# Performance work log

Hardware: AMD Instinct MI355X
Metric: run time of the kernel (lower is better)

## Reference

```python
import jax, jax.numpy as jnp
import numpy as np
from jax import lax

B_SZ, D_SPEC, P, NC, MLP_D = 4096, 30, 9, 64, 64
L = P * P + 1  # 82 tokens (81 spiral + cls)


def _spiral_idx(patch=P):
    # Replicates Scan.forward's hardcoded assignments_map: center pixel, then
    # concentric rings (top row, right col, bottom row, left col), each of length 2r.
    cen = patch // 2
    rows, cols = [cen], [cen]
    for r in range(1, cen + 1):
        rows += [cen - r] * (2 * r); cols += list(range(cen - r + 1, cen + r + 1))
        rows += list(range(cen - r + 1, cen + r + 1)); cols += [cen + r] * (2 * r)
        rows += [cen + r] * (2 * r); cols += list(range(cen - r, cen + r))
        rows += list(range(cen - r, cen + r)); cols += [cen - r] * (2 * r)
    return np.asarray(rows), np.asarray(cols)

_ROWS, _COLS = _spiral_idx()


def _ln(x, g, b, eps=1e-5):
    m = x.mean(-1, keepdims=True)
    v = ((x - m) ** 2).mean(-1, keepdims=True)
    return (x - m) * lax.rsqrt(v + eps) * g + b


def _bn(x, g, b, m, v, nspatial, eps=1e-5):
    sh = (1, -1) + (1,) * nspatial
    return (x - m.reshape(sh)) * lax.rsqrt(v.reshape(sh) + eps) * g.reshape(sh) + b.reshape(sh)


def setup_inputs():
    key = jax.random.key(0)
    ks = iter(jax.random.split(key, 40))
    def rn(shape, s=0.1):
        return s * jax.random.normal(next(ks), shape, jnp.float32)
    return {
        "input_data": jax.random.normal(next(ks), (B_SZ, 1, D_SPEC, P, P), jnp.float32),
        "w3": rn((8, 1, 3, 3, 3)), "b3": rn((8,)),
        "g3": 1.0 + rn((8,)), "be3": rn((8,)), "m3": jnp.zeros((8,)), "v3": jnp.ones((8,)),
        "w2c": rn((NC, 8 * D_SPEC, 3, 3)), "b2c": rn((NC,)),
        "g2": 1.0 + rn((NC,)), "be2": rn((NC,)), "m2": jnp.zeros((NC,)), "v2": jnp.ones((NC,)),
        "pos_emb": rn((1, L, NC)), "cls_tok": rn((1, 1, NC)),
        "ln1_g": jnp.ones((NC,)), "ln1_b": jnp.zeros((NC,)),
        "Wb": rn((NC, NC)), "bb": rn((NC,)),
        "Wc": rn((NC, NC)), "bc": rn((NC,)),
        "Wd": rn((NC, NC)), "bd": rn((NC,)),
        "delta_p": rn((1, L, NC)), "A_p": rn((L, NC)),
        "Wst": rn((NC, NC)), "bst": rn((NC,)), "bias_st": rn((1, 1, NC)),
        "ln2_g": jnp.ones((NC,)), "ln2_b": jnp.zeros((NC,)),
        "Wm1": rn((NC, MLP_D)), "bm1": rn((MLP_D,)),
        "Wm2": rn((MLP_D, NC)), "bm2": rn((NC,)),
    }


def _forward(input_data, w3, b3, g3, be3, m3, v3, w2c, b2c, g2, be2, m2, v2,
             pos_emb, cls_tok, ln1_g, ln1_b, Wb, bb, Wc, bc, Wd, bd,
             delta_p, A_p, Wst, bst, bias_st, ln2_g, ln2_b, Wm1, bm1, Wm2, bm2):
    b = input_data.shape[0]
    # conv3d (SAME, k=3) + BN(eval) + ReLU
    h = lax.conv_general_dilated(input_data, w3, (1, 1, 1), [(1, 1)] * 3,
                                 dimension_numbers=("NCDHW", "OIDHW", "NCDHW"))
    h = jax.nn.relu(_bn(h + b3[None, :, None, None, None], g3, be3, m3, v3, 3))
    h = h.reshape(b, 8 * D_SPEC, P, P)  # 'b c h w y -> b (c h) w y'
    # conv2d (SAME, k=3) + BN(eval) + ReLU
    h = lax.conv_general_dilated(h, w2c, (1, 1), [(1, 1)] * 2,
                                 dimension_numbers=("NCHW", "OIHW", "NCHW"))
    h = jax.nn.relu(_bn(h + b2c[None, :, None, None], g2, be2, m2, v2, 2))
    # spiral scan gather: [B,C,H,W] -> [B,81,C]
    seq = jnp.transpose(h, (0, 2, 3, 1))[:, _ROWS, _COLS, :]
    tok = jnp.concatenate([jnp.broadcast_to(cls_tok, (b, 1, NC)), seq], axis=1) + pos_emb
    # (emb dropout = identity in eval)
    # --- Residual(LayerNormalize(S6_noC)) ---
    xn = _ln(tok, ln1_g, ln1_b)
    z = jax.nn.sigmoid(xn)
    B0 = xn @ Wb + bb
    C_ = xn @ Wc + bc
    sq = jnp.mean(xn, axis=1, keepdims=True)              # SToken squeeze [B,1,D]
    sq = jax.nn.sigmoid(jax.nn.relu(sq @ Wst + bst))
    T_ = (sq + bias_st) * xn                              # [B,L,D]
    delta = jax.nn.sigmoid(xn @ Wd + bd + delta_p)
    A_ = delta * A_p[None]                                # [B,L,D]
    Bx = delta * B0 * xn                                  # B_ * x fused
    def step(s, inp):
        a, bx, c, t = inp
        s = a * s + bx
        return s, c * s + t
    ins = (jnp.moveaxis(A_, 1, 0), jnp.moveaxis(Bx, 1, 0),
           jnp.moveaxis(C_, 1, 0), jnp.moveaxis(T_, 1, 0))  # [L,B,D]
    _, out = lax.scan(step, jnp.zeros((b, NC), xn.dtype), ins)
    tok = tok + jnp.moveaxis(out, 0, 1) * z               # residual
    # AdaptiveAvgPool1d(1) over seq + squeeze -> [B, D]
    pooled = tok.mean(axis=1)
    # --- Residual(LayerNormalize(MLP_Block)) (dropout = identity) ---
    yn = _ln(pooled, ln2_g, ln2_b)
    mlp = jax.nn.gelu(yn @ Wm1 + bm1, approximate=False) @ Wm2 + bm2
    return pooled + mlp


def reference(input_data, w3, b3, g3, be3, m3, v3, w2c, b2c, g2, be2, m2, v2,
              pos_emb, cls_tok, ln1_g, ln1_b, Wb, bb, Wc, bc, Wd, bd,
              delta_p, A_p, Wst, bst, bias_st, ln2_g, ln2_b, Wm1, bm1, Wm2, bm2):
    return _forward(input_data, w3, b3, g3, be3, m3, v3, w2c, b2c, g2, be2, m2, v2,
                    pos_emb, cls_tok, ln1_g, ln1_b, Wb, bb, Wc, bc, Wd, bd,
                    delta_p, A_p, Wst, bst, bias_st, ln2_g, ln2_b, Wm1, bm1, Wm2, bm2)
```

## Files before the change

### kernel.cpp

```cpp
#include <hip/hip_runtime.h>

typedef unsigned short u16;
typedef unsigned int u32;
typedef __attribute__((ext_vector_type(8))) short bf16x8;
typedef __attribute__((ext_vector_type(4))) float f32x4;
typedef __attribute__((ext_vector_type(4))) int i32x4;

#define DEV __device__ __forceinline__

DEV u16 f2bf(float f){
  unsigned u = __float_as_uint(f);
  u += 0x7fffu + ((u >> 16) & 1u);
  return (u16)(u >> 16);
}
DEV float bf2f(u16 h){ return __uint_as_float(((unsigned)h) << 16); }

DEV int spiral_t(int pix){
  int px = pix / 9, py = pix % 9;
  int dr = px - 4, dc = py - 4;
  int ar = dr < 0 ? -dr : dr, ac = dc < 0 ? -dc : dc;
  int r = ar > ac ? ar : ac;
  if (r == 0) return 0;
  int start = 1 + 4*r*(r-1);
  if (dr == -r && dc >= -r+1) return start + dc + r - 1;
  if (dc == r)  return start + 2*r + dr + r - 1;
  if (dr == r)  return start + 4*r + dc + r;
  return start + 6*r + dr + r;
}

__global__ __launch_bounds__(256) void k_conv3d(const float* __restrict__ x,
    const float* __restrict__ w3, const float* __restrict__ b3,
    const float* __restrict__ g3, const float* __restrict__ be3,
    const float* __restrict__ m3, const float* __restrict__ v3,
    const float* __restrict__ w2c, const float* __restrict__ g2,
    const float* __restrict__ v2,
    u16* __restrict__ h1, u16* __restrict__ Wt2){
  __shared__ float tile[3993];
  __shared__ float wle[216];
  __shared__ float sc[8], sh[8];
  int b = blockIdx.x, tid = threadIdx.x;

  if (b >= 4096){
    int idx = (b - 4096)*256 + tid;
    int kk = idx & 31;
    int o  = (idx >> 5) & 63;
    int tile2 = idx >> 11;
    int dxy = tile2 >> 3;
    int chunk = tile2 & 7;
    int ch = chunk*32 + kk;
    float v = 0.f;
    if (ch < 240){
      float s2 = g2[o] * rsqrtf(v2[o] + 1e-5f);
      v = w2c[(o*240 + ch)*9 + dxy] * s2;
    }
    Wt2[idx] = f2bf(v);
    return;
  }

  for (int i = tid; i < 3993; i += 256) tile[i] = 0.f;
  if (tid < 216) wle[tid] = w3[tid];
  if (tid < 8){
    float s = g3[tid]*rsqrtf(v3[tid]+1e-5f);
    sc[tid] = s;
    sh[tid] = (b3[tid]-m3[tid])*s + be3[tid];
  }
  __syncthreads();
  const float* xin = x + b*2430;
  for (int i = tid; i < 2430; i += 256){
    int dd = i / 81, rem = i % 81;
    int px = rem / 9, py = rem % 9;
    tile[(dd+1)*121 + (px+1)*11 + (py+1)] = xin[i];
  }
  __syncthreads();
  u16* hb = h1 + (size_t)b*19440;

  for (int col = tid; col < 648; col += 256){
    int pix = col >> 3, co = col & 7;
    int px = pix / 9, py = pix % 9;
    const float* base = tile + px*11 + py;
    float wp[27];
    #pragma unroll
    for (int q=0;q<27;q++) wp[q] = wle[co*27+q];
    float scv = sc[co], shv = sh[co];

    float s0[9], s1[9], s2[9];
#define LSL(S, SL)                                                            \
    { const float* tp2 = base + (SL)*121;                                     \
      _Pragma("unroll")                                                       \
      for (int kx=0;kx<3;kx++)                                                \
        _Pragma("unroll")                                                     \
        for (int ky=0;ky<3;ky++) S[kx*3+ky] = tp2[kx*11+ky]; }
#define DOT3(A, SA, SB, SC)                                                   \
    { A = 0.f;                                                                \
      _Pragma("unroll")                                                       \
      for (int q=0;q<9;q++) A = fmaf(SA[q], wp[q], A);                        \
      _Pragma("unroll")                                                       \
      for (int q=0;q<9;q++) A = fmaf(SB[q], wp[9+q], A);                      \
      _Pragma("unroll")                                                       \
      for (int q=0;q<9;q++) A = fmaf(SC[q], wp[18+q], A); }

    LSL(s0, 0); LSL(s1, 1); LSL(s2, 2);
    u16 outv[30];
    #pragma unroll
    for (int d3 = 0; d3 < 30; d3 += 3){
      float a;
      DOT3(a, s0, s1, s2);
      outv[d3] = f2bf(fmaxf(fmaf(a, scv, shv), 0.f));
      LSL(s0, d3+3);
      DOT3(a, s1, s2, s0);
      outv[d3+1] = f2bf(fmaxf(fmaf(a, scv, shv), 0.f));
      LSL(s1, d3+4);
      DOT3(a, s2, s0, s1);
      outv[d3+2] = f2bf(fmaxf(fmaf(a, scv, shv), 0.f));
      LSL(s2, d3+5);
    }
#undef LSL
#undef DOT3
    u32* dst = (u32*)(hb + pix*240 + co*30);
    #pragma unroll
    for (int q=0;q<15;q++) dst[q] = ((u32)outv[2*q+1] << 16) | (u32)outv[2*q];
  }
}

__global__ __launch_bounds__(256, 2) void k_conv2d(const u16* __restrict__ h1,
    const u16* __restrict__ Wt2,
    const float* __restrict__ b2c, const float* __restrict__ g2,
    const float* __restrict__ be2, const float* __restrict__ m2,
    const float* __restrict__ v2,
    const float* __restrict__ pos_emb, const float* __restrict__ cls_tok,
    const float* __restrict__ ln1_g, const float* __restrict__ ln1_b,
    const float* __restrict__ Wst, const float* __restrict__ bst,
    const float* __restrict__ bias_st,
    u16* __restrict__ xn, float* __restrict__ tsum, float* __restrict__ sqs){
  __shared__ __align__(16) char smem[80848];
  const int ZROW = 80352;
  int tid = threadIdx.x;
  int wv = tid >> 6, ln = tid & 63;
  int lq = ln >> 4, lr = ln & 15;
  int img0 = blockIdx.x*2;
  size_t grow0 = (size_t)img0*81;

  int bln = lr*32 + lq*8;

#define LOADB(TAP, C, B)                                                        \
    { const u16* Bt_ = Wt2 + (TAP)*16384 + bln;                                 \
      _Pragma("unroll")                                                         \
      for (int kk=0;kk<2;kk++)                                                  \
        _Pragma("unroll")                                                       \
        for (int j=0;j<4;j++)                                                   \
          B[kk][j] = *(const bf16x8*)(Bt_ + ((C)*2+kk)*2048 + j*512); }

  bf16x8 bB0[2][4], bB1[2][4], bB2[2][4];
  LOADB(0, 0, bB0);
  LOADB(0, 1, bB1);
  LOADB(0, 2, bB2);

  for (int r = tid; r < 162; r += 256)
    *(i32x4*)(smem + r*496 + 480) = (i32x4){0,0,0,0};
  if (tid < 31) *(i32x4*)(smem + ZROW + tid*16) = (i32x4){0,0,0,0};
  {
    const u16* src = h1 + grow0*240;
    for (int idx = tid; idx < 162*30; idx += 256){
      int r = idx / 30, c = idx % 30;
      *(i32x4*)(smem + r*496 + c*16) = *(const i32x4*)(src + idx*8);
    }
  }
  __syncthreads();

  f32x4 acc[3][4];
  #pragma unroll
  for (int i=0;i<3;i++)
    #pragma unroll
    for (int j=0;j<4;j++) acc[i][j] = (f32x4){0.f,0.f,0.f,0.f};

#define CALCADDR(TAP, A0, A1, A13)                                              \
  { int dx = (TAP)/3 - 1, dy = (TAP)%3 - 1;                                     \
    _Pragma("unroll")                                                           \
    for (int rt=0;rt<3;rt++){                                                   \
      int row = (wv*3+rt)*16 + lr;                                              \
      int pix = row % 81;                                                       \
      int px = pix/9, py = pix%9;                                               \
      int px2 = px + dx, py2 = py + dy;                                         \
      bool valid = (row < 162) && ((unsigned)px2 < 9u) && ((unsigned)py2 < 9u); \
      int nrow = (row - pix) + px2*9 + py2;                                     \
      int base = valid ? nrow*496 : ZROW;                                       \
      A0[rt]  = base + lq*16;                                                   \
      A1[rt]  = base + 64 + lq*16;                                              \
      A13[rt] = (lq == 3) ? ZROW : (A1[rt] + 384);                              \
    } }

#define LOADA(C, SA0, SA1, SA13, A0, A1)                                        \
    { _Pragma("unroll")                                                         \
      for (int rt=0;rt<3;rt++){                                                 \
        A0[rt] = *(const bf16x8*)(smem + SA0[rt] + (C)*128);                    \
        A1[rt] = *(const bf16x8*)(smem + ((C)==3 ? SA13[rt]                     \
                                                 : SA1[rt] + (C)*128)); } }

#define DOMFMA(B, A0, A1)                                                       \
    { __builtin_amdgcn_s_setprio(1);                                            \
      _Pragma("unroll")                                                         \
      for (int rt=0;rt<3;rt++)                                                  \
        _Pragma("unroll")                                                       \
        for (int j=0;j<4;j++)                                                   \
          acc[rt][j] = __builtin_amdgcn_mfma_f32_16x16x32_bf16(A0[rt], B[0][j], acc[rt][j], 0, 0, 0); \
      _Pragma("unroll")                                                         \
      for (int rt=0;rt<3;rt++)                                                  \
        _Pragma("unroll")                                                       \
        for (int j=0;j<4;j++)                                                   \
          acc[rt][j] = __builtin_amdgcn_mfma_f32_16x16x32_bf16(A1[rt], B[1][j], acc[rt][j], 0, 0, 0); \
      __builtin_amdgcn_s_setprio(0); }

#define TAPBODY(TAPV, BA, BB, BC)                                               \
  { int ntap_ = (TAPV) < 8 ? (TAPV)+1 : 8;                                      \
    DOMFMA(BA, aAX0, aAX1);                                                     \
    LOADB((TAPV), 3, BA); LOADA(2, aC0, aC1, aC13, aAX0, aAX1);                 \
    DOMFMA(BB, aAY0, aAY1);                                                     \
    LOADB(ntap_, 0, BB); CALCADDR(ntap_, aN0, aN1, aN13);                       \
    LOADA(3, aC0, aC1, aC13, aAY0, aAY1);                                       \
    DOMFMA(BC, aAX0, aAX1);                                                     \
    LOADB(ntap_, 1, BC); LOADA(0, aN0, aN1, aN13, aAX0, aAX1);                  \
    DOMFMA(BA, aAY0, aAY1);                                                     \
    LOADB(ntap_, 2, BA); LOADA(1, aN0, aN1, aN13, aAY0, aAY1);                  \
    _Pragma("unroll")                                                           \
    for (int rt=0;rt<3;rt++){ aC0[rt]=aN0[rt]; aC1[rt]=aN1[rt]; aC13[rt]=aN13[rt]; } }

  int aC0[3], aC1[3], aC13[3];
  int aN0[3], aN1[3], aN13[3];
  bf16x8 aAX0[3], aAX1[3], aAY0[3], aAY1[3];

  CALCADDR(0, aC0, aC1, aC13);
  LOADA(0, aC0, aC1, aC13, aAX0, aAX1);
  LOADA(1, aC0, aC1, aC13, aAY0, aAY1);

  for (int t3 = 0; t3 < 9; t3 += 3){
    TAPBODY(t3+0, bB0, bB1, bB2);
    TAPBODY(t3+1, bB1, bB2, bB0);
    TAPBODY(t3+2, bB2, bB0, bB1);
  }
#undef CALCADDR
#undef LOADB
#undef LOADA
#undef DOMFMA
#undef TAPBODY

  __syncthreads();

  float t2c[4], lg[4], lb[4];
  #pragma unroll
  for (int j=0;j<4;j++){
    int col = j*16 + lr;
    float s2 = g2[col]*rsqrtf(v2[col]+1e-5f);
    t2c[j] = (b2c[col]-m2[col])*s2 + be2[col];
    lg[j] = ln1_g[col]; lb[j] = ln1_b[col];
  }

  float st0[4]={0,0,0,0}, st1[4]={0,0,0,0};
  float sx0[4]={0,0,0,0}, sx1[4]={0,0,0,0};

  #pragma unroll
  for (int rt=0;rt<3;rt++){
    #pragma unroll
    for (int e=0;e<4;e++){
      int row = (wv*3+rt)*16 + lq*4 + e;
      if (row < 162){
        int im = (row >= 81);
        int pix = row - im*81;
        int tsp = spiral_t(pix);
        const float* pe = pos_emb + (1+tsp)*64;
        float y[4], m1 = 0.f, m2v = 0.f;
        #pragma unroll
        for (int j=0;j<4;j++){
          y[j] = fmaxf(acc[rt][j][e] + t2c[j], 0.f) + pe[j*16+lr];
          m1 += y[j]; m2v = fmaf(y[j], y[j], m2v);
        }
        #pragma unroll
        for (int off=1; off<16; off<<=1){
          m1  += __shfl_xor(m1,  off, 64);
          m2v += __shfl_xor(m2v, off, 64);
        }
        float mean = m1*(1.f/64.f);
        float var  = m2v*(1.f/64.f) - mean*mean;
        float rs = rsqrtf(var + 1e-5f);
        u16* dst = xn + ((size_t)(img0+im)*82 + 1 + tsp)*64;
        #pragma unroll
        for (int j=0;j<4;j++){
          float xnv = (y[j]-mean)*rs*lg[j] + lb[j];
          dst[j*16+lr] = f2bf(xnv);
          if (im == 0){ st0[j] += y[j]; sx0[j] += xnv; }
          else        { st1[j] += y[j]; sx1[j] += xnv; }
        }
      }
    }
  }

  #pragma unroll
  for (int j=0;j<4;j++){
    st0[j] += __shfl_xor(st0[j],16,64); st0[j] += __shfl_xor(st0[j],32,64);
    st1[j] += __shfl_xor(st1[j],16,64); st1[j] += __shfl_xor(st1[j],32,64);
    sx0[j] += __shfl_xor(sx0[j],16,64); sx0[j] += __shfl_xor(sx0[j],32,64);
    sx1[j] += __shfl_xor(sx1[j],16,64); sx1[j] += __shfl_xor(sx1[j],32,64);
  }
  float* partT = (float*)smem;
  float* partX = (float*)(smem + 2048);
  float* xsumL = (float*)(smem + 4096);
  if (lq == 0){
    #pragma unroll
    for (int j=0;j<4;j++){
      partT[wv*128 +       j*16+lr] = st0[j];
      partT[wv*128 + 64  + j*16+lr] = st1[j];
      partX[wv*128 +       j*16+lr] = sx0[j];
      partX[wv*128 + 64  + j*16+lr] = sx1[j];
    }
  }
  __syncthreads();
  if (tid < 128){
    int im = tid >> 6, d = tid & 63;
    float tt = partT[im*64+d] + partT[128+im*64+d] + partT[256+im*64+d] + partT[384+im*64+d];
    float xx = partX[im*64+d] + partX[128+im*64+d] + partX[256+im*64+d] + partX[384+im*64+d];
    float clsv = cls_tok[d] + pos_emb[d];
    float c1v = clsv, c2v = clsv*clsv;
    #pragma unroll
    for (int off=1; off<64; off<<=1){ c1v += __shfl_xor(c1v, off, 64); c2v += __shfl_xor(c2v, off, 64); }
    float cm = c1v*(1.f/64.f), cv = c2v*(1.f/64.f) - cm*cm;
    float cxn = (clsv - cm)*rsqrtf(cv + 1e-5f)*ln1_g[d] + ln1_b[d];
    xn[((size_t)(img0+im)*82)*64 + d] = f2bf(cxn);
    tsum[(size_t)(img0+im)*64 + d] = tt + clsv;
    xsumL[im*64 + d] = (xx + cxn) * (1.f/82.f);
  }
  __syncthreads();
  {
    int im = tid >> 7, d2 = tid & 127;
    int d = d2 >> 1, half = d2 & 1;
    float a = 0.f;
    int k0 = half*32;
    #pragma unroll
    for (int k=0;k<32;k++) a = fmaf(xsumL[im*64 + k0+k], Wst[(k0+k)*64+d], a);
    a += __shfl_xor(a, 1, 64);
    if (half == 0){
      a += bst[d];
      a = fmaxf(a, 0.f);
      a = 1.f/(1.f + __expf(-a));
      sqs[(size_t)(img0+im)*64 + d] = a + bias_st[d];
    }
  }
}

__global__ __launch_bounds__(256, 2) void k_fuse(const u16* __restrict__ xn,
    const float* __restrict__ tsum, const float* __restrict__ sqs,
    const float* __restrict__ Wb, const float* __restrict__ Wc, const float* __restrict__ Wd,
    const float* __restrict__ bbv, const float* __restrict__ bcv, const float* __restrict__ bdv,
    const float* __restrict__ delta_p, const float* __restrict__ A_p,
    const float* __restrict__ ln2_g, const float* __restrict__ ln2_b,
    const float* __restrict__ Wm1, const float* __restrict__ bm1,
    const float* __restrict__ Wm2, const float* __restrict__ bm2,
    float* __restrict__ out){
  __shared__ __align__(16) char xnL[96*128];
  __shared__ u16 AxL[96][66], BxL[96][66], CxL[96][66];
  int tid = threadIdx.x;
  int wv = tid >> 6, ln = tid & 63;
  int lq = ln >> 4, lr = ln & 15;
  int b = blockIdx.x;

  bf16x8 bfr[3][2];
  {
    int cc = wv*16 + lr;
    const float* Ws[3] = {Wb, Wc, Wd};
    #pragma unroll
    for (int w=0;w<3;w++)
      #pragma unroll
      for (int kk=0;kk<2;kk++){
        int k0 = kk*32 + lq*8;
        bf16x8 f;
        #pragma unroll
        for (int e=0;e<8;e++) f[e] = (short)f2bf(Ws[w][(k0+e)*64 + cc]);
        bfr[w][kk] = f;
      }
  }

  {
    const u16* src = xn + (size_t)b*82*64;
    for (int idx = tid; idx < 656; idx += 256){
      int r = idx >> 3, c = idx & 7;
      *(i32x4*)(xnL + r*128 + ((c*16) ^ ((r&7)<<4))) = *(const i32x4*)(src + idx*8);
    }
    for (int idx = tid; idx < 112; idx += 256){
      int r = 82 + (idx >> 3), c = idx & 7;
      *(i32x4*)(xnL + r*128 + ((c*16) ^ ((r&7)<<4))) = (i32x4){0,0,0,0};
    }
  }
  __syncthreads();

  f32x4 acc[6][3];
  #pragma unroll
  for (int i=0;i<6;i++)
    #pragma unroll
    for (int w=0;w<3;w++) acc[i][w] = (f32x4){0.f,0.f,0.f,0.f};

  #pragma unroll
  for (int rt=0;rt<6;rt++){
    int row = rt*16 + lr;
    bf16x8 afr[2];
    #pragma unroll
    for (int kk=0;kk<2;kk++)
      afr[kk] = *(const bf16x8*)(xnL + row*128 + ((kk*64 + lq*16) ^ ((row&7)<<4)));
    #pragma unroll
    for (int kk=0;kk<2;kk++)
      #pragma unroll
      for (int w=0;w<3;w++)
        acc[rt][w] = __builtin_amdgcn_mfma_f32_16x16x32_bf16(afr[kk], bfr[w][kk], acc[rt][w], 0, 0, 0);
  }

  {
    int d = wv*16 + lr;
    float bB = bbv[d], bC = bcv[d], bD = bdv[d];
    #pragma unroll
    for (int rt=0;rt<6;rt++){
      #pragma unroll
      for (int e=0;e<4;e++){
        int t = rt*16 + lq*4 + e;
        if (t < 82){
          float B0 = acc[rt][0][e] + bB;
          float Cv = acc[rt][1][e] + bC;
          float Dr = acc[rt][2][e] + bD + delta_p[t*64+d];
          float D  = 1.f/(1.f + __expf(-Dr));
          float xv = bf2f(*(const u16*)(xnL + t*128 + ((d*2) ^ ((t&7)<<4))));
          AxL[t][d] = f2bf(D * A_p[t*64+d]);
          BxL[t][d] = f2bf(D * B0 * xv);
          CxL[t][d] = f2bf(Cv);
        }
      }
    }
  }
  __syncthreads();

  if (wv == 0){
    int d = ln;
    float sq = sqs[(size_t)b*64 + d];
    float s = 0.f, racc = 0.f;
    for (int t = 0; t < 82; t++){
      float a  = bf2f(AxL[t][d]);
      float bx = bf2f(BxL[t][d]);
      float c  = bf2f(CxL[t][d]);
      float xv = bf2f(*(const u16*)(xnL + t*128 + ((d*2) ^ ((t&7)<<4))));
      s = fmaf(a, s, bx);
      float o = fmaf(c, s, sq*xv);
      float z = 1.f/(1.f + __expf(-xv));
      racc = fmaf(o, z, racc);
    }
    float pooled = (tsum[(size_t)b*64 + d] + racc) * (1.f/82.f);
    float s1 = pooled, s2v = pooled*pooled;
    #pragma unroll
    for (int off=32; off>0; off>>=1){ s1 += __shfl_xor(s1, off, 64); s2v += __shfl_xor(s2v, off, 64); }
    float mean = s1*(1.f/64.f), var = s2v*(1.f/64.f) - mean*mean;
    float yn = (pooled - mean)*rsqrtf(var + 1e-5f)*ln2_g[d] + ln2_b[d];
    float a1 = bm1[d];
    for (int k=0;k<64;k++) a1 = fmaf(__shfl(yn, k, 64), Wm1[k*64+d], a1);
    float hg = 0.5f*a1*(1.f + erff(a1*0.70710678118654752f));
    float a2 = bm2[d];
    for (int k=0;k<64;k++) a2 = fmaf(__shfl(hg, k, 64), Wm2[k*64+d], a2);
    out[(size_t)b*64 + d] = pooled + a2;
  }
}

extern "C" void kernel_launch(void* const* d_in, const int* in_sizes, int n_in,
                              void* d_out, int out_size, void* d_ws, size_t ws_size,
                              hipStream_t stream){
  const float* x       = (const float*)d_in[0];
  const float* w3      = (const float*)d_in[1];
  const float* b3      = (const float*)d_in[2];
  const float* g3      = (const float*)d_in[3];
  const float* be3     = (const float*)d_in[4];
  const float* m3      = (const float*)d_in[5];
  const float* v3      = (const float*)d_in[6];
  const float* w2c     = (const float*)d_in[7];
  const float* b2c     = (const float*)d_in[8];
  const float* g2      = (const float*)d_in[9];
  const float* be2     = (const float*)d_in[10];
  const float* m2      = (const float*)d_in[11];
  const float* v2      = (const float*)d_in[12];
  const float* pos_emb = (const float*)d_in[13];
  const float* cls_tok = (const float*)d_in[14];
  const float* ln1_g   = (const float*)d_in[15];
  const float* ln1_b   = (const float*)d_in[16];
  const float* Wb      = (const float*)d_in[17];
  const float* bbv     = (const float*)d_in[18];
  const float* Wc      = (const float*)d_in[19];
  const float* bc      = (const float*)d_in[20];
  const float* Wd      = (const float*)d_in[21];
  const float* bd      = (const float*)d_in[22];
  const float* delta_p = (const float*)d_in[23];
  const float* A_p     = (const float*)d_in[24];
  const float* Wst     = (const float*)d_in[25];
  const float* bst     = (const float*)d_in[26];
  const float* bias_st = (const float*)d_in[27];
  const float* ln2_g   = (const float*)d_in[28];
  const float* ln2_b   = (const float*)d_in[29];
  const float* Wm1     = (const float*)d_in[30];
  const float* bm1     = (const float*)d_in[31];
  const float* Wm2     = (const float*)d_in[32];
  const float* bm2     = (const float*)d_in[33];

  char* ws = (char*)d_ws;
  u16*   h1   = (u16*)ws;
  u16*   Wt2  = (u16*)(ws + 159252480);
  u16*   xnb  = (u16*)(ws + 159571968);
  float* tsum = (float*)(ws + 202563584);
  float* sqs  = (float*)(ws + 203612160);

  k_conv3d<<<4672, 256, 0, stream>>>(x, w3, b3, g3, be3, m3, v3,
                                     w2c, g2, v2, h1, Wt2);
  k_conv2d<<<2048, 256, 0, stream>>>(h1, Wt2, b2c, g2, be2, m2, v2,
                                     pos_emb, cls_tok, ln1_g, ln1_b,
                                     Wst, bst, bias_st, xnb, tsum, sqs);
  k_fuse  <<<4096, 256, 0, stream>>>(xnb, tsum, sqs, Wb, Wc, Wd, bbv, bc, bd,
                                     delta_p, A_p, ln2_g, ln2_b,
                                     Wm1, bm1, Wm2, bm2, (float*)d_out);
}
```

Baseline: 359.3 us.

## Split conv2d K dimension across wave pairs with LDS reduction

Result: slower. 608.0 us (+69.2%).

```diff
diff --git a/kernel.cpp b/kernel.cpp
--- a/kernel.cpp
+++ b/kernel.cpp
@@ -122,7 +122,7 @@
   }
 }
 
-__global__ __launch_bounds__(256, 2) void k_conv2d(const u16* __restrict__ h1,
+__global__ __launch_bounds__(256, 1) void k_conv2d(const u16* __restrict__ h1,
     const u16* __restrict__ Wt2,
     const float* __restrict__ b2c, const float* __restrict__ g2,
     const float* __restrict__ be2, const float* __restrict__ m2,
@@ -137,10 +137,12 @@
   int tid = threadIdx.x;
   int wv = tid >> 6, ln = tid & 63;
   int lq = ln >> 4, lr = ln & 15;
+  int p = wv >> 1, q = wv & 1;
   int img0 = blockIdx.x*2;
   size_t grow0 = (size_t)img0*81;
 
   int bln = lr*32 + lq*8;
+  int c0 = q*2, c1 = q*2 + 1;
 
 #define LOADB(TAP, C, B)                                                        \
     { const u16* Bt_ = Wt2 + (TAP)*16384 + bln;                                 \
@@ -150,10 +152,9 @@
         for (int j=0;j<4;j++)                                                   \
           B[kk][j] = *(const bf16x8*)(Bt_ + ((C)*2+kk)*2048 + j*512); }
 
-  bf16x8 bB0[2][4], bB1[2][4], bB2[2][4];
-  LOADB(0, 0, bB0);
-  LOADB(0, 1, bB1);
-  LOADB(0, 2, bB2);
+  bf16x8 bA[2][4], bB[2][4];
+  LOADB(0, c0, bA);
+  LOADB(0, c1, bB);
 
   for (int r = tid; r < 162; r += 256)
     *(i32x4*)(smem + r*496 + 480) = (i32x4){0,0,0,0};
@@ -167,82 +168,90 @@
   }
   __syncthreads();
 
-  f32x4 acc[3][4];
-  #pragma unroll
-  for (int i=0;i<3;i++)
+  f32x4 acc[6][4];
+  #pragma unroll
+  for (int i=0;i<6;i++)
     #pragma unroll
     for (int j=0;j<4;j++) acc[i][j] = (f32x4){0.f,0.f,0.f,0.f};
 
-#define CALCADDR(TAP, A0, A1, A13)                                              \
+  int aC0[6], aC1[6];
+  bf16x8 afr[6][2];
+
+#define CALCADDR(TAP)                                                           \
   { int dx = (TAP)/3 - 1, dy = (TAP)%3 - 1;                                     \
     _Pragma("unroll")                                                           \
-    for (int rt=0;rt<3;rt++){                                                   \
-      int row = (wv*3+rt)*16 + lr;                                              \
+    for (int rt=0;rt<6;rt++){                                                   \
+      int row = p*96 + rt*16 + lr;                                              \
       int pix = row % 81;                                                       \
       int px = pix/9, py = pix%9;                                               \
       int px2 = px + dx, py2 = py + dy;                                         \
       bool valid = (row < 162) && ((unsigned)px2 < 9u) && ((unsigned)py2 < 9u); \
       int nrow = (row - pix) + px2*9 + py2;                                     \
       int base = valid ? nrow*496 : ZROW;                                       \
-      A0[rt]  = base + lq*16;                                                   \
-      A1[rt]  = base + 64 + lq*16;                                              \
-      A13[rt] = (lq == 3) ? ZROW : (A1[rt] + 384);                              \
+      aC0[rt] = base + lq*16;                                                   \
+      aC1[rt] = base + 64 + lq*16;                                              \
     } }
 
-#define LOADA(C, SA0, SA1, SA13, A0, A1)                                        \
+#define LOADA1(RT, C)                                                           \
+    { afr[RT][0] = *(const bf16x8*)(smem + aC0[RT] + (C)*128);                  \
+      int a1a_ = ((C)==3) ? ((lq==3) ? ZROW : aC1[RT] + 384)                    \
+                          : (aC1[RT] + (C)*128);                                \
+      afr[RT][1] = *(const bf16x8*)(smem + a1a_); }
+
+#define GROUP(B, NC)                                                            \
     { _Pragma("unroll")                                                         \
-      for (int rt=0;rt<3;rt++){                                                 \
-        A0[rt] = *(const bf16x8*)(smem + SA0[rt] + (C)*128);                    \
-        A1[rt] = *(const bf16x8*)(smem + ((C)==3 ? SA13[rt]                     \
-                                                 : SA1[rt] + (C)*128)); } }
-
-#define DOMFMA(B, A0, A1)                                                       \
-    { __builtin_amdgcn_s_setprio(1);                                            \
-      _Pragma("unroll")                                                         \
-      for (int rt=0;rt<3;rt++)                                                  \
+      for (int rt=0;rt<6;rt++){                                                 \
+        __builtin_amdgcn_s_setprio(1);                                          \
         _Pragma("unroll")                                                       \
         for (int j=0;j<4;j++)                                                   \
-          acc[rt][j] = __builtin_amdgcn_mfma_f32_16x16x32_bf16(A0[rt], B[0][j], acc[rt][j], 0, 0, 0); \
-      _Pragma("unroll")                                                         \
-      for (int rt=0;rt<3;rt++)                                                  \
+          acc[rt][j] = __builtin_amdgcn_mfma_f32_16x16x32_bf16(afr[rt][0], B[0][j], acc[rt][j], 0, 0, 0); \
         _Pragma("unroll")                                                       \
         for (int j=0;j<4;j++)                                                   \
-          acc[rt][j] = __builtin_amdgcn_mfma_f32_16x16x32_bf16(A1[rt], B[1][j], acc[rt][j], 0, 0, 0); \
-      __builtin_amdgcn_s_setprio(0); }
-
-#define TAPBODY(TAPV, BA, BB, BC)                                               \
-  { int ntap_ = (TAPV) < 8 ? (TAPV)+1 : 8;                                      \
-    DOMFMA(BA, aAX0, aAX1);                                                     \
-    LOADB((TAPV), 3, BA); LOADA(2, aC0, aC1, aC13, aAX0, aAX1);                 \
-    DOMFMA(BB, aAY0, aAY1);                                                     \
-    LOADB(ntap_, 0, BB); CALCADDR(ntap_, aN0, aN1, aN13);                       \
-    LOADA(3, aC0, aC1, aC13, aAY0, aAY1);                                       \
-    DOMFMA(BC, aAX0, aAX1);                                                     \
-    LOADB(ntap_, 1, BC); LOADA(0, aN0, aN1, aN13, aAX0, aAX1);                  \
-    DOMFMA(BA, aAY0, aAY1);                                                     \
-    LOADB(ntap_, 2, BA); LOADA(1, aN0, aN1, aN13, aAY0, aAY1);                  \
-    _Pragma("unroll")                                                           \
-    for (int rt=0;rt<3;rt++){ aC0[rt]=aN0[rt]; aC1[rt]=aN1[rt]; aC13[rt]=aN13[rt]; } }
-
-  int aC0[3], aC1[3], aC13[3];
-  int aN0[3], aN1[3], aN13[3];
-  bf16x8 aAX0[3], aAX1[3], aAY0[3], aAY1[3];
-
-  CALCADDR(0, aC0, aC1, aC13);
-  LOADA(0, aC0, aC1, aC13, aAX0, aAX1);
-  LOADA(1, aC0, aC1, aC13, aAY0, aAY1);
-
-  for (int t3 = 0; t3 < 9; t3 += 3){
-    TAPBODY(t3+0, bB0, bB1, bB2);
-    TAPBODY(t3+1, bB1, bB2, bB0);
-    TAPBODY(t3+2, bB2, bB0, bB1);
+          acc[rt][j] = __builtin_amdgcn_mfma_f32_16x16x32_bf16(afr[rt][1], B[1][j], acc[rt][j], 0, 0, 0); \
+        __builtin_amdgcn_s_setprio(0);                                          \
+        LOADA1(rt, NC);                                                         \
+      } }
+
+  CALCADDR(0);
+  #pragma unroll
+  for (int rt=0;rt<6;rt++){ LOADA1(rt, c0); }
+
+  for (int tap = 0; tap < 9; tap++){
+    int ntap = (tap < 8) ? tap + 1 : 8;
+    GROUP(bA, c1);
+    LOADB(ntap, c0, bA);
+    CALCADDR(ntap);
+    GROUP(bB, c0);
+    LOADB(ntap, c1, bB);
   }
 #undef CALCADDR
 #undef LOADB
-#undef LOADA
-#undef DOMFMA
-#undef TAPBODY
-
+#undef LOADA1
+#undef GROUP
+
+  __syncthreads();
+  float* ex = (float*)smem;
+  int rtw0 = q ? 0 : 3;
+  #pragma unroll
+  for (int k=0;k<3;k++){
+    int rt = rtw0 + k;
+    #pragma unroll
+    for (int e=0;e<4;e++)
+      #pragma unroll
+      for (int j=0;j<4;j++)
+        ex[p*6144 + (rt*16 + lq*4 + e)*64 + j*16 + lr] = acc[rt][j][e];
+  }
+  __syncthreads();
+  int rtr0 = q ? 3 : 0;
+  #pragma unroll
+  for (int k=0;k<3;k++){
+    int rt = rtr0 + k;
+    #pragma unroll
+    for (int e=0;e<4;e++)
+      #pragma unroll
+      for (int j=0;j<4;j++)
+        acc[rt][j][e] += ex[p*6144 + (rt*16 + lq*4 + e)*64 + j*16 + lr];
+  }
   __syncthreads();
 
   float t2c[4], lg[4], lb[4];
@@ -258,10 +267,11 @@
   float sx0[4]={0,0,0,0}, sx1[4]={0,0,0,0};
 
   #pragma unroll
-  for (int rt=0;rt<3;rt++){
+  for (int k=0;k<3;k++){
+    int rt = rtr0 + k;
     #pragma unroll
     for (int e=0;e<4;e++){
-      int row = (wv*3+rt)*16 + lq*4 + e;
+      int row = p*96 + rt*16 + lq*4 + e;
       if (row < 162){
         int im = (row >= 81);
         int pix = row - im*81;
```

## Fuse selective-scan and MLP stage into conv2d kernel via shared memory

Applied to the files above, without the earlier changes.

Measured after the change: 361.7 us. Within noise of the previous version (+0.7%).

```diff
diff --git a/kernel.cpp b/kernel.cpp
--- a/kernel.cpp
+++ b/kernel.cpp
@@ -131,9 +131,19 @@
     const float* __restrict__ ln1_g, const float* __restrict__ ln1_b,
     const float* __restrict__ Wst, const float* __restrict__ bst,
     const float* __restrict__ bias_st,
-    u16* __restrict__ xn, float* __restrict__ tsum, float* __restrict__ sqs){
+    const float* __restrict__ Wb, const float* __restrict__ Wc,
+    const float* __restrict__ Wd,
+    const float* __restrict__ bbv, const float* __restrict__ bcv,
+    const float* __restrict__ bdv,
+    const float* __restrict__ delta_p, const float* __restrict__ A_p,
+    const float* __restrict__ ln2_g, const float* __restrict__ ln2_b,
+    const float* __restrict__ Wm1, const float* __restrict__ bm1,
+    const float* __restrict__ Wm2, const float* __restrict__ bm2,
+    float* __restrict__ out){
   __shared__ __align__(16) char smem[80848];
   const int ZROW = 80352;
+  const int TSUML = 24576, SQSL = 25088, AXo = 25600, BXo = 38272, CXo = 50944;
+  const int PTo = 63616, PXo = 65664, XSo = 67712;
   int tid = threadIdx.x;
   int wv = tid >> 6, ln = tid & 63;
   int lq = ln >> 4, lr = ln & 15;
@@ -244,6 +254,12 @@
 #undef TAPBODY
 
   __syncthreads();
+
+  if (tid < 224){
+    int im = tid / 112, r2 = tid % 112;
+    int rr = 82 + (r2 >> 3), c = r2 & 7;
+    *(i32x4*)(smem + im*12288 + rr*128 + ((c*16) ^ ((rr&7)<<4))) = (i32x4){0,0,0,0};
+  }
 
   float t2c[4], lg[4], lb[4];
   #pragma unroll
@@ -281,11 +297,13 @@
         float mean = m1*(1.f/64.f);
         float var  = m2v*(1.f/64.f) - mean*mean;
         float rs = rsqrtf(var + 1e-5f);
-        u16* dst = xn + ((size_t)(img0+im)*82 + 1 + tsp)*64;
+        int trow = 1 + tsp;
+        char* dl = smem + im*12288 + trow*128;
+        int sz = (trow & 7) << 4;
         #pragma unroll
         for (int j=0;j<4;j++){
           float xnv = (y[j]-mean)*rs*lg[j] + lb[j];
-          dst[j*16+lr] = f2bf(xnv);
+          *(u16*)(dl + (((j*16+lr)*2) ^ sz)) = f2bf(xnv);
           if (im == 0){ st0[j] += y[j]; sx0[j] += xnv; }
           else        { st1[j] += y[j]; sx1[j] += xnv; }
         }
@@ -300,9 +318,11 @@
     sx0[j] += __shfl_xor(sx0[j],16,64); sx0[j] += __shfl_xor(sx0[j],32,64);
     sx1[j] += __shfl_xor(sx1[j],16,64); sx1[j] += __shfl_xor(sx1[j],32,64);
   }
-  float* partT = (float*)smem;
-  float* partX = (float*)(smem + 2048);
-  float* xsumL = (float*)(smem + 4096);
+  float* partT = (float*)(smem + PTo);
+  float* partX = (float*)(smem + PXo);
+  float* xsumL = (float*)(smem + XSo);
+  float* tsumL = (float*)(smem + TSUML);
+  float* sqsL  = (float*)(smem + SQSL);
   if (lq == 0){
     #pragma unroll
     for (int j=0;j<4;j++){
@@ -323,8 +343,8 @@
     for (int off=1; off<64; off<<=1){ c1v += __shfl_xor(c1v, off, 64); c2v += __shfl_xor(c2v, off, 64); }
     float cm = c1v*(1.f/64.f), cv = c2v*(1.f/64.f) - cm*cm;
     float cxn = (clsv - cm)*rsqrtf(cv + 1e-5f)*ln1_g[d] + ln1_b[d];
-    xn[((size_t)(img0+im)*82)*64 + d] = f2bf(cxn);
-    tsum[(size_t)(img0+im)*64 + d] = tt + clsv;
+    *(u16*)(smem + im*12288 + d*2) = f2bf(cxn);
+    tsumL[im*64 + d] = tt + clsv;
     xsumL[im*64 + d] = (xx + cxn) * (1.f/82.f);
   }
   __syncthreads();
@@ -340,26 +360,10 @@
       a += bst[d];
       a = fmaxf(a, 0.f);
       a = 1.f/(1.f + __expf(-a));
-      sqs[(size_t)(img0+im)*64 + d] = a + bias_st[d];
-    }
-  }
-}
-
-__global__ __launch_bounds__(256, 2) void k_fuse(const u16* __restrict__ xn,
-    const float* __restrict__ tsum, const float* __restrict__ sqs,
-    const float* __restrict__ Wb, const float* __restrict__ Wc, const float* __restrict__ Wd,
-    const float* __restrict__ bbv, const float* __restrict__ bcv, const float* __restrict__ bdv,
-    const float* __restrict__ delta_p, const float* __restrict__ A_p,
-    const float* __restrict__ ln2_g, const float* __restrict__ ln2_b,
-    const float* __restrict__ Wm1, const float* __restrict__ bm1,
-    const float* __restrict__ Wm2, const float* __restrict__ bm2,
-    float* __restrict__ out){
-  __shared__ __align__(16) char xnL[96*128];
-  __shared__ u16 AxL[96][66], BxL[96][66], CxL[96][66];
-  int tid = threadIdx.x;
-  int wv = tid >> 6, ln = tid & 63;
-  int lq = ln >> 4, lr = ln & 15;
-  int b = blockIdx.x;
+      sqsL[im*64 + d] = a + bias_st[d];
+    }
+  }
+  __syncthreads();
 
   bf16x8 bfr[3][2];
   {
@@ -376,89 +380,83 @@
         bfr[w][kk] = f;
       }
   }
-
-  {
-    const u16* src = xn + (size_t)b*82*64;
-    for (int idx = tid; idx < 656; idx += 256){
-      int r = idx >> 3, c = idx & 7;
-      *(i32x4*)(xnL + r*128 + ((c*16) ^ ((r&7)<<4))) = *(const i32x4*)(src + idx*8);
-    }
-    for (int idx = tid; idx < 112; idx += 256){
-      int r = 82 + (idx >> 3), c = idx & 7;
-      *(i32x4*)(xnL + r*128 + ((c*16) ^ ((r&7)<<4))) = (i32x4){0,0,0,0};
-    }
-  }
-  __syncthreads();
-
-  f32x4 acc[6][3];
-  #pragma unroll
-  for (int i=0;i<6;i++)
-    #pragma unroll
-    for (int w=0;w<3;w++) acc[i][w] = (f32x4){0.f,0.f,0.f,0.f};
-
-  #pragma unroll
-  for (int rt=0;rt<6;rt++){
-    int row = rt*16 + lr;
-    bf16x8 afr[2];
-    #pragma unroll
-    for (int kk=0;kk<2;kk++)
-      afr[kk] = *(const bf16x8*)(xnL + row*128 + ((kk*64 + lq*16) ^ ((row&7)<<4)));
-    #pragma unroll
-    for (int kk=0;kk<2;kk++)
+  u16* AxL = (u16*)(smem + AXo);
+  u16* BxL = (u16*)(smem + BXo);
+  u16* CxL = (u16*)(smem + CXo);
+
+  for (int im = 0; im < 2; im++){
+    const char* xb = smem + im*12288;
+    f32x4 facc[6][3];
+    #pragma unroll
+    for (int i=0;i<6;i++)
       #pragma unroll
-      for (int w=0;w<3;w++)
-        acc[rt][w] = __builtin_amdgcn_mfma_f32_16x16x32_bf16(afr[kk], bfr[w][kk], acc[rt][w], 0, 0, 0);
-  }
-
-  {
-    int d = wv*16 + lr;
-    float bB = bbv[d], bC = bcv[d], bD = bdv[d];
+      for (int w=0;w<3;w++) facc[i][w] = (f32x4){0.f,0.f,0.f,0.f};
+
     #pragma unroll
     for (int rt=0;rt<6;rt++){
+      int row = rt*16 + lr;
+      bf16x8 afr[2];
       #pragma unroll
-      for (int e=0;e<4;e++){
-        int t = rt*16 + lq*4 + e;
-        if (t < 82){
-          float B0 = acc[rt][0][e] + bB;
-          float Cv = acc[rt][1][e] + bC;
-          float Dr = acc[rt][2][e] + bD + delta_p[t*64+d];
-          float D  = 1.f/(1.f + __expf(-Dr));
-          float xv = bf2f(*(const u16*)(xnL + t*128 + ((d*2) ^ ((t&7)<<4))));
-          AxL[t][d] = f2bf(D * A_p[t*64+d]);
-          BxL[t][d] = f2bf(D * B0 * xv);
-          CxL[t][d] = f2bf(Cv);
+      for (int kk=0;kk<2;kk++)
+        afr[kk] = *(const bf16x8*)(xb + row*128 + ((kk*64 + lq*16) ^ ((row&7)<<4)));
+      #pragma unroll
+      for (int kk=0;kk<2;kk++)
+        #pragma unroll
+        for (int w=0;w<3;w++)
+          facc[rt][w] = __builtin_amdgcn_mfma_f32_16x16x32_bf16(afr[kk], bfr[w][kk], facc[rt][w], 0, 0, 0);
+    }
+
+    {
+      int d = wv*16 + lr;
+      float bB = bbv[d], bC = bcv[d], bD = bdv[d];
+      #pragma unroll
+      for (int rt=0;rt<6;rt++){
+        #pragma unroll
+        for (int e=0;e<4;e++){
+          int t = rt*16 + lq*4 + e;
+          if (t < 82){
+            float B0 = facc[rt][0][e] + bB;
+            float Cv = facc[rt][1][e] + bC;
+            float Dr = facc[rt][2][e] + bD + delta_p[t*64+d];
+            float D  = 1.f/(1.f + __expf(-Dr));
+            float xv = bf2f(*(const u16*)(xb + t*128 + ((d*2) ^ ((t&7)<<4))));
+            AxL[t*66+d] = f2bf(D * A_p[t*64+d]);
+            BxL[t*66+d] = f2bf(D * B0 * xv);
+            CxL[t*66+d] = f2bf(Cv);
+          }
         }
       }
     }
-  }
-  __syncthreads();
-
-  if (wv == 0){
-    int d = ln;
-    float sq = sqs[(size_t)b*64 + d];
-    float s = 0.f, racc = 0.f;
-    for (int t = 0; t < 82; t++){
-      float a  = bf2f(AxL[t][d]);
-      float bx = bf2f(BxL[t][d]);
-      float c  = bf2f(CxL[t][d]);
-      float xv = bf2f(*(const u16*)(xnL + t*128 + ((d*2) ^ ((t&7)<<4))));
-      s = fmaf(a, s, bx);
-      float o = fmaf(c, s, sq*xv);
-      float z = 1.f/(1.f + __expf(-xv));
-      racc = fmaf(o, z, racc);
-    }
-    float pooled = (tsum[(size_t)b*64 + d] + racc) * (1.f/82.f);
-    float s1 = pooled, s2v = pooled*pooled;
-    #pragma unroll
-    for (int off=32; off>0; off>>=1){ s1 += __shfl_xor(s1, off, 64); s2v += __shfl_xor(s2v, off, 64); }
-    float mean = s1*(1.f/64.f), var = s2v*(1.f/64.f) - mean*mean;
-    float yn = (pooled - mean)*rsqrtf(var + 1e-5f)*ln2_g[d] + ln2_b[d];
-    float a1 = bm1[d];
-    for (int k=0;k<64;k++) a1 = fmaf(__shfl(yn, k, 64), Wm1[k*64+d], a1);
-    float hg = 0.5f*a1*(1.f + erff(a1*0.70710678118654752f));
-    float a2 = bm2[d];
-    for (int k=0;k<64;k++) a2 = fmaf(__shfl(hg, k, 64), Wm2[k*64+d], a2);
-    out[(size_t)b*64 + d] = pooled + a2;
+    __syncthreads();
+
+    if (wv == 0){
+      int d = ln;
+      float sq = sqsL[im*64 + d];
+      float s = 0.f, racc = 0.f;
+      for (int t = 0; t < 82; t++){
+        float a  = bf2f(AxL[t*66+d]);
+        float bx = bf2f(BxL[t*66+d]);
+        float c  = bf2f(CxL[t*66+d]);
+        float xv = bf2f(*(const u16*)(xb + t*128 + ((d*2) ^ ((t&7)<<4))));
+        s = fmaf(a, s, bx);
+        float o = fmaf(c, s, sq*xv);
+        float z = 1.f/(1.f + __expf(-xv));
+        racc = fmaf(o, z, racc);
+      }
+      float pooled = (tsumL[im*64 + d] + racc) * (1.f/82.f);
+      float s1 = pooled, s2v = pooled*pooled;
+      #pragma unroll
+      for (int off=32; off>0; off>>=1){ s1 += __shfl_xor(s1, off, 64); s2v += __shfl_xor(s2v, off, 64); }
+      float mean = s1*(1.f/64.f), var = s2v*(1.f/64.f) - mean*mean;
+      float yn = (pooled - mean)*rsqrtf(var + 1e-5f)*ln2_g[d] + ln2_b[d];
+      float a1 = bm1[d];
+      for (int k=0;k<64;k++) a1 = fmaf(__shfl(yn, k, 64), Wm1[k*64+d], a1);
+      float hg = 0.5f*a1*(1.f + erff(a1*0.70710678118654752f));
+      float a2 = bm2[d];
+      for (int k=0;k<64;k++) a2 = fmaf(__shfl(hg, k, 64), Wm2[k*64+d], a2);
+      out[(size_t)(img0+im)*64 + d] = pooled + a2;
+    }
+    __syncthreads();
   }
 }
 
@@ -503,16 +501,13 @@
   char* ws = (char*)d_ws;
   u16*   h1   = (u16*)ws;
   u16*   Wt2  = (u16*)(ws + 159252480);
-  u16*   xnb  = (u16*)(ws + 159571968);
-  float* tsum = (float*)(ws + 202563584);
-  float* sqs  = (float*)(ws + 203612160);
 
   k_conv3d<<<4672, 256, 0, stream>>>(x, w3, b3, g3, be3, m3, v3,
                                      w2c, g2, v2, h1, Wt2);
   k_conv2d<<<2048, 256, 0, stream>>>(h1, Wt2, b2c, g2, be2, m2, v2,
                                      pos_emb, cls_tok, ln1_g, ln1_b,
-                                     Wst, bst, bias_st, xnb, tsum, sqs);
-  k_fuse  <<<4096, 256, 0, stream>>>(xnb, tsum, sqs, Wb, Wc, Wd, bbv, bc, bd,
-                                     delta_p, A_p, ln2_g, ln2_b,
-                                     Wm1, bm1, Wm2, bm2, (float*)d_out);
+                                     Wst, bst, bias_st,
+                                     Wb, Wc, Wd, bbv, bc, bd, delta_p, A_p,
+                                     ln2_g, ln2_b, Wm1, bm1, Wm2, bm2,
+                                     (float*)d_out);
 }
```
